# Optimization experiments

Hardware: AMD Instinct MI355X
Metric: run time of the kernel (lower is better)

The kernel has to match this reference:

```python
import jax, jax.numpy as jnp
import numpy as np

B, S, F = 64, 512, 1024
D_MODEL, D_MEM, D_IN, H, D_OUT, N_SYNC, T, H_NLM = 2048, 32, 1024, 16, 1000, 512, 16, 32
DH = D_IN // H


def _ln(x, g, b):
    m = x.mean(-1, keepdims=True)
    v = ((x - m) ** 2).mean(-1, keepdims=True)
    return (x - m) * jax.lax.rsqrt(v + 1e-5) * g + b


def setup_inputs() -> dict:
    key = jax.random.key(0)
    ks = jax.random.split(key, 24)
    def n(i, shape, fan):
        return jax.random.normal(ks[i], shape, jnp.float32) * (fan ** -0.5)
    u = 1.0 / np.sqrt(D_MODEL)
    uh = 1.0 / np.sqrt(D_MODEL + D_MEM)
    return dict(
        x=jax.random.normal(ks[0], (B, S, F), jnp.float32),
        W_kv=n(1, (F, D_IN), F), b_kv=jnp.zeros((D_IN,)),
        g_kv=jnp.ones((D_IN,)), be_kv=jnp.zeros((D_IN,)),
        W_q=n(2, (N_SYNC, D_IN), N_SYNC), b_q=jnp.zeros((D_IN,)),
        W_aq=n(3, (D_IN, D_IN), D_IN), b_aq=jnp.zeros((D_IN,)),
        W_ak=n(4, (D_IN, D_IN), D_IN), b_ak=jnp.zeros((D_IN,)),
        W_av=n(5, (D_IN, D_IN), D_IN), b_av=jnp.zeros((D_IN,)),
        W_ao=n(6, (D_IN, D_IN), D_IN), b_ao=jnp.zeros((D_IN,)),
        W_s1=n(7, (D_IN + D_MODEL, D_MODEL), D_IN + D_MODEL), b_s1=jnp.zeros((D_MODEL,)),
        W_s2=n(8, (D_MODEL, D_MODEL), D_MODEL), b_s2=jnp.zeros((D_MODEL,)),
        g_s=jnp.ones((D_MODEL,)), be_s=jnp.zeros((D_MODEL,)),
        W_n1=n(9, (D_MODEL, D_MEM, H_NLM), D_MEM), b_n1=jnp.zeros((D_MODEL, H_NLM)),
        W_n2=n(10, (D_MODEL, H_NLM), H_NLM), b_n2=jnp.zeros((D_MODEL,)),
        g_n=jnp.ones((D_MODEL,)), be_n=jnp.zeros((D_MODEL,)),
        init_state=jax.random.uniform(ks[11], (D_MODEL,), jnp.float32, -u, u),
        init_hist=jax.random.uniform(ks[12], (D_MODEL, D_MEM), jnp.float32, -uh, uh),
        decay_action=jax.random.uniform(ks[13], (N_SYNC,), jnp.float32, 0.0, 2.0),
        decay_out=jax.random.uniform(ks[14], (N_SYNC,), jnp.float32, 0.0, 2.0),
        W_out=n(15, (N_SYNC, D_OUT), N_SYNC), b_out=jnp.zeros((D_OUT,)),
        idx_la=jax.random.randint(ks[16], (N_SYNC,), 0, D_MODEL),
        idx_ra=jax.random.randint(ks[17], (N_SYNC,), 0, D_MODEL),
        idx_lo=jax.random.randint(ks[18], (N_SYNC,), 0, D_MODEL),
        idx_ro=jax.random.randint(ks[19], (N_SYNC,), 0, D_MODEL),
    )


def reference(x, W_kv, b_kv, g_kv, be_kv, W_q, b_q, W_aq, b_aq, W_ak, b_ak,
              W_av, b_av, W_ao, b_ao, W_s1, b_s1, W_s2, b_s2, g_s, be_s,
              W_n1, b_n1, W_n2, b_n2, g_n, be_n, init_state, init_hist,
              decay_action, decay_out, W_out, b_out,
              idx_la, idx_ra, idx_lo, idx_ro):
    # kv features: Linear + LayerNorm, fixed across ticks -> project k,v once
    kv = _ln(x @ W_kv + b_kv, g_kv, be_kv)                      # (B,S,D_IN)
    kh = (kv @ W_ak + b_ak).reshape(B, S, H, DH)
    vh = (kv @ W_av + b_av).reshape(B, S, H, DH)
    # learnable exponential decay r = exp(-clamp(p,0,15))
    rA = jnp.exp(-jnp.clip(decay_action, 0.0, 15.0))[None, :]
    rO = jnp.exp(-jnp.clip(decay_out, 0.0, 15.0))[None, :]
    act0 = jnp.broadcast_to(init_state, (B, D_MODEL))
    hist0 = jnp.broadcast_to(init_hist, (B, D_MODEL, D_MEM))
    # out-sync initialized before loop (None branch): alpha=prod, beta=1
    aO0 = act0[:, idx_lo] * act0[:, idx_ro]
    bO0 = jnp.ones_like(aO0)
    # action-sync None branch at tick0 == recurrence from alpha=beta=0
    aA0 = jnp.zeros((B, N_SYNC), x.dtype)
    bA0 = jnp.zeros((B, N_SYNC), x.dtype)

    def step(carry, _):
        act, hist, aA, bA, aO, bO = carry
        pA = act[:, idx_la] * act[:, idx_ra]                    # paired-neuron gather
        aA = rA * aA + pA
        bA = rA * bA + 1.0
        sync_a = aA * jax.lax.rsqrt(bA)
        q = sync_a @ W_q + b_q                                  # (B,D_IN)
        qh = (q @ W_aq + b_aq).reshape(B, H, DH)
        attn_w = jax.nn.softmax(jnp.einsum('bhd,bshd->bhs', qh, kh) / np.sqrt(DH), axis=-1)
        attn = jnp.einsum('bhs,bshd->bhd', attn_w, vh).reshape(B, D_IN) @ W_ao + b_ao
        pre = jnp.concatenate([attn, act], axis=-1)             # (B, D_IN+D_MODEL)
        pre_act = _ln(jax.nn.gelu(pre @ W_s1 + b_s1) @ W_s2 + b_s2, g_s, be_s)
        hist = jnp.concatenate([hist[:, :, 1:], pre_act[:, :, None]], axis=-1)
        # per-neuron deep NLM over the memory window
        hmid = jax.nn.relu(jnp.einsum('bdm,dmh->bdh', hist, W_n1) + b_n1)
        act = _ln(jnp.einsum('bdh,dh->bd', hmid, W_n2) + b_n2, g_n, be_n)
        pO = act[:, idx_lo] * act[:, idx_ro]
        aO = rO * aO + pO
        bO = rO * bO + 1.0
        pred = (aO * jax.lax.rsqrt(bO)) @ W_out + b_out         # (B,D_OUT)
        logp = jax.nn.log_softmax(pred, axis=-1)
        ne = -(jnp.exp(logp) * logp).sum(-1) / np.log(D_OUT)    # normalized entropy
        return (act, hist, aA, bA, aO, bO), (pred, ne)

    _, (preds, nes) = jax.lax.scan(step, (act0, hist0, aA0, bA0, aO0, bO0), None, length=T)
    predictions = jnp.transpose(preds, (1, 2, 0))               # (B,D_OUT,T)
    certainties = jnp.transpose(jnp.stack([nes, 1.0 - nes], axis=1), (2, 1, 0))  # (B,2,T)
    return predictions, certainties
```

## Files before the change

kernel.cpp:

```cpp
#include <hip/hip_runtime.h>
#include <hip/hip_bf16.h>


#define B_ 64
#define S_ 512
#define F_ 1024
#define DMODEL 2048
#define DMEM 32
#define DIN 1024
#define NH 16
#define DH 64
#define DOUT 1000
#define NSYNC 512
#define TICKS 16
#define HNLM 32
#define HIST_W 48

typedef __attribute__((ext_vector_type(8))) short short8;
typedef __attribute__((ext_vector_type(4))) float f32x4;

__device__ inline void store_f(float* p, float v) { *p = v; }
__device__ inline void store_f(__hip_bfloat16* p, float v) { *p = __float2bfloat16(v); }

__device__ inline short f2bs(float f) {
  __hip_bfloat16 h = __float2bfloat16(f);
  return *reinterpret_cast<short*>(&h);
}

__device__ inline float bfs(short x) {
  return __uint_as_float(((unsigned)(unsigned short)x) << 16);
}

__device__ inline float gelu_f(float x) {
  float x3 = x * x * x;
  return 0.5f * x * (1.f + tanhf(0.7978845608028654f * (x + 0.044715f * x3)));
}

__device__ inline float bf_lo(unsigned v) { return __uint_as_float(v << 16); }
__device__ inline float bf_hi(unsigned v) { return __uint_as_float(v & 0xffff0000u); }

__global__ __launch_bounds__(256) void transpose_bf16_kernel(const float* __restrict__ W,
                                                             __hip_bfloat16* __restrict__ Wt,
                                                             int K, int N, int Npad, int ldw,
                                                             int koff) {
  __shared__ float t[32][33];
  const int tx = threadIdx.x, ty = threadIdx.y;
  const int n0 = blockIdx.x * 32, k0 = blockIdx.y * 32;
#pragma unroll
  for (int i = 0; i < 4; i++) {
    int k = k0 + ty + i * 8;
    t[ty + i * 8][tx] = (k < K && n0 + tx < N) ? W[(size_t)k * N + n0 + tx] : 0.f;
  }
  __syncthreads();
#pragma unroll
  for (int i = 0; i < 4; i++) {
    int n = n0 + ty + i * 8;
    if (n < Npad && k0 + tx < K)
      Wt[(size_t)n * ldw + koff + k0 + tx] = __float2bfloat16(t[tx][ty + i * 8]);
  }
}

__global__ void conv_bf16_kernel(const float* __restrict__ src, __hip_bfloat16* __restrict__ dst,
                                 int n) {
  int i = blockIdx.x * 256 + threadIdx.x;
  if (i < n) dst[i] = __float2bfloat16(src[i]);
}

__global__ void bqaq_kernel(const float* __restrict__ b_q, const float* __restrict__ b_aq,
                            const __hip_bfloat16* __restrict__ Wt_aq, float* __restrict__ b_qaq) {
  int n = blockIdx.x * 256 + threadIdx.x;
  if (n >= DIN) return;
  const __hip_bfloat16* wr = Wt_aq + (size_t)n * DIN;
  float s = b_aq[n];
  for (int k = 0; k < DIN; k++) s += b_q[k] * __bfloat162float(wr[k]);
  b_qaq[n] = s;
}

__global__ void bs1c_kernel(const float* __restrict__ b_s1, const float* __restrict__ b_ao,
                            const float* __restrict__ W_s1, float* __restrict__ b_s1c) {
  int n = blockIdx.x * 256 + threadIdx.x;
  if (n >= DMODEL) return;
  float s = b_s1[n];
  for (int k = 0; k < DIN; k++) s += b_ao[k] * W_s1[(size_t)k * DMODEL + n];
  b_s1c[n] = s;
}

__device__ inline short8 load_chunk(const __hip_bfloat16* p) {
  return *reinterpret_cast<const short8*>(p);
}
__device__ inline short8 load_chunk(const float* p) {
  short8 r;
#pragma unroll
  for (int j = 0; j < 8; j++) r[j] = f2bs(p[j]);
  return r;
}

template <int TRANSC, typename TA, typename TC>
__global__ __launch_bounds__(256) void gemm_big(const TA* __restrict__ A,
                                                const __hip_bfloat16* __restrict__ Bt,
                                                const float* __restrict__ bias,
                                                TC* __restrict__ C, int M, int N, int K) {
  __shared__ short lsA[128 * 64];
  __shared__ short lsB[128 * 64];
  const int tid = threadIdx.x;
  const int l = tid & 63, w = tid >> 6;
  const int wr = (w >> 1) * 64, wc = (w & 1) * 64;
  const int nwg = gridDim.x * gridDim.y;
  const int flat = blockIdx.y * gridDim.x + blockIdx.x;
  const int wk = (flat & 7) * (nwg >> 3) + (flat >> 3);
  const int brow = (wk / gridDim.x) * 128, bcol = (wk % gridDim.x) * 128;
  f32x4 acc[4][4];
#pragma unroll
  for (int i = 0; i < 4; i++)
#pragma unroll
    for (int j = 0; j < 4; j++)
#pragma unroll
      for (int r = 0; r < 4; r++) acc[i][j][r] = 0.f;

  short8 ra[4], rb[4];
  auto gload = [&](int k0) {
#pragma unroll
    for (int q = 0; q < 4; q++) {
      int i = tid + q * 256;
      int row = i >> 3, c = i & 7;
      ra[q] = load_chunk(A + (size_t)(brow + row) * K + k0 + c * 8);
      rb[q] = load_chunk(Bt + (size_t)(bcol + row) * K + k0 + c * 8);
    }
  };
  auto lwrite = [&]() {
#pragma unroll
    for (int q = 0; q < 4; q++) {
      int i = tid + q * 256;
      int row = i >> 3, c = i & 7;
      int sw = c ^ (row & 7);
      *reinterpret_cast<short8*>(&lsA[row * 64 + sw * 8]) = ra[q];
      *reinterpret_cast<short8*>(&lsB[row * 64 + sw * 8]) = rb[q];
    }
  };
  gload(0);
  for (int k0 = 0; k0 < K; k0 += 64) {
    __syncthreads();
    lwrite();
    if (k0 + 64 < K) gload(k0 + 64);
    __syncthreads();
#pragma unroll
    for (int ks = 0; ks < 2; ks++) {
      short8 af[4], bfv[4];
#pragma unroll
      for (int mi = 0; mi < 4; mi++) {
        int row = wr + mi * 16 + (l & 15);
        int c = ks * 4 + (l >> 4);
        af[mi] = *reinterpret_cast<const short8*>(&lsA[row * 64 + (c ^ (row & 7)) * 8]);
      }
#pragma unroll
      for (int ni = 0; ni < 4; ni++) {
        int row = wc + ni * 16 + (l & 15);
        int c = ks * 4 + (l >> 4);
        bfv[ni] = *reinterpret_cast<const short8*>(&lsB[row * 64 + (c ^ (row & 7)) * 8]);
      }
#pragma unroll
      for (int mi = 0; mi < 4; mi++)
#pragma unroll
        for (int ni = 0; ni < 4; ni++)
          acc[mi][ni] =
              __builtin_amdgcn_mfma_f32_16x16x32_bf16(af[mi], bfv[ni], acc[mi][ni], 0, 0, 0);
    }
  }
#pragma unroll
  for (int mi = 0; mi < 4; mi++)
#pragma unroll
    for (int ni = 0; ni < 4; ni++)
#pragma unroll
      for (int r = 0; r < 4; r++) {
        int row = brow + wr + mi * 16 + (l >> 4) * 4 + r;
        int col = bcol + wc + ni * 16 + (l & 15);
        float v = acc[mi][ni][r];
        if (bias) v += bias[col];
        if (TRANSC == 1) {
          store_f(&C[(size_t)col * M + row], v);
        } else if (TRANSC == 2) {
          int bb = row >> 9, s = row & 511, hh = col >> 6, dd = col & 63;
          store_f(&C[(((size_t)(bb * 16 + hh) * 512) + s) * 64 + dd], v);
        } else {
          store_f(&C[(size_t)row * N + col], v);
        }
      }
}

template <typename TOUT>
__global__ __launch_bounds__(256) void ln_kernel(const float* __restrict__ x,
                                                 const float* __restrict__ g,
                                                 const float* __restrict__ be,
                                                 TOUT* __restrict__ out, int C,
                                                 size_t row_stride, int col_stride) {
  const int row = blockIdx.x;
  const int tid = threadIdx.x;
  const float* xr = x + (size_t)row * C;
  float s = 0.f, s2 = 0.f;
  for (int c = tid; c < C; c += 256) {
    float v = xr[c];
    s += v;
    s2 += v * v;
  }
  __shared__ float r1[256], r2[256];
  r1[tid] = s;
  r2[tid] = s2;
  __syncthreads();
  for (int st = 128; st > 0; st >>= 1) {
    if (tid < st) {
      r1[tid] += r1[tid + st];
      r2[tid] += r2[tid + st];
    }
    __syncthreads();
  }
  float mean = r1[0] / C;
  float var = r2[0] / C - mean * mean;
  float inv = 1.0f / sqrtf(var + 1e-5f);
  for (int c = tid; c < C; c += 256) {
    float v = (xr[c] - mean) * inv * g[c] + be[c];
    store_f(&out[(size_t)row * row_stride + (size_t)c * col_stride], v);
  }
}

__global__ void init_pre_kernel(const float* __restrict__ init_state,
                                __hip_bfloat16* __restrict__ pre) {
  int i = blockIdx.x * 256 + threadIdx.x;
  if (i >= B_ * DMODEL) return;
  int b = i >> 11, j = i & (DMODEL - 1);
  pre[(size_t)b * 3072 + DIN + j] = __float2bfloat16(init_state[j]);
}

__global__ void init_hist_kernel(const float* __restrict__ init_hist, float* __restrict__ hist) {
  int i = blockIdx.x * 256 + threadIdx.x;
  if (i >= B_ * DMODEL * DMEM) return;
  int m = i & (DMEM - 1);
  int bd = i >> 5;
  int d = bd & (DMODEL - 1);
  hist[(size_t)bd * HIST_W + m] = init_hist[d * DMEM + m];
}

__global__ void init_sync_kernel(const float* __restrict__ init_state,
                                 const float* __restrict__ decay_action,
                                 const float* __restrict__ decay_out,
                                 const int* __restrict__ la, const int* __restrict__ ra,
                                 const int* __restrict__ lo, const int* __restrict__ ro,
                                 float* __restrict__ aA, float* __restrict__ bA,
                                 float* __restrict__ aO, float* __restrict__ bO,
                                 float* __restrict__ syncA0, float* __restrict__ rAv,
                                 float* __restrict__ rOv) {
  int i = blockIdx.x * 256 + threadIdx.x;
  if (i >= B_ * NSYNC) return;
  int j = i & (NSYNC - 1);
  if (i < NSYNC) {
    rAv[i] = expf(-fminf(fmaxf(decay_action[i], 0.f), 15.f));
    rOv[i] = expf(-fminf(fmaxf(decay_out[i], 0.f), 15.f));
  }
  float pA = init_state[la[j]] * init_state[ra[j]];
  aA[i] = pA;
  bA[i] = 1.f;
  syncA0[i] = pA;
  aO[i] = init_state[lo[j]] * init_state[ro[j]];
  bO[i] = 1.f;
}

__global__ __launch_bounds__(256) void qh0_kernel(const float* __restrict__ syncA0,
                                                  const __hip_bfloat16* __restrict__ Wt_qaq,
                                                  const float* __restrict__ b_qaq,
                                                  float* __restrict__ qhb) {
  __shared__ float sa[512];
  const int b = blockIdx.x;
  const int tid = threadIdx.x;
  sa[tid] = syncA0[(size_t)b * NSYNC + tid];
  sa[tid + 256] = syncA0[(size_t)b * NSYNC + 256 + tid];
  __syncthreads();
#pragma unroll
  for (int i = 0; i < 4; i++) {
    int n = tid + i * 256;
    const unsigned* wr = reinterpret_cast<const unsigned*>(Wt_qaq + (size_t)n * NSYNC);
    float s = b_qaq[n];
    for (int c = 0; c < 256; c++) {
      unsigned uu = wr[c];
      s += sa[2 * c] * bf_lo(uu) + sa[2 * c + 1] * bf_hi(uu);
    }
    qhb[(size_t)b * DIN + n] = s;
  }
}

template <typename EPI>
__device__ __forceinline__ void mm_tile64(const __hip_bfloat16* __restrict__ A, int lda,
                                          const __hip_bfloat16* __restrict__ Bt, int ldb,
                                          int bcol, int kb, int kchunk, int tid, short* lsA,
                                          short* lsB, EPI epi) {
  const int l = tid & 63, w = tid >> 6;
  f32x4 acc[4];
#pragma unroll
  for (int i = 0; i < 4; i++)
#pragma unroll
    for (int r = 0; r < 4; r++) acc[i][r] = 0.f;
  short8 ra[2], rb[2];
  auto gload = [&](int k0) {
#pragma unroll
    for (int q = 0; q < 2; q++) {
      int i = tid + q * 256;
      int row = i >> 3, c = i & 7;
      ra[q] = *reinterpret_cast<const short8*>(A + (size_t)row * lda + k0 + c * 8);
      rb[q] = *reinterpret_cast<const short8*>(Bt + (size_t)(bcol + row) * ldb + k0 + c * 8);
    }
  };
  auto lwrite = [&]() {
#pragma unroll
    for (int q = 0; q < 2; q++) {
      int i = tid + q * 256;
      int row = i >> 3, c = i & 7;
      int sw = c ^ (row & 7);
      *reinterpret_cast<short8*>(&lsA[row * 64 + sw * 8]) = ra[q];
      *reinterpret_cast<short8*>(&lsB[row * 64 + sw * 8]) = rb[q];
    }
  };
  gload(kb);
  for (int k0 = kb; k0 < kb + kchunk; k0 += 64) {
    __syncthreads();
    lwrite();
    if (k0 + 64 < kb + kchunk) gload(k0 + 64);
    __syncthreads();
#pragma unroll
    for (int ks = 0; ks < 2; ks++) {
      int rowa = w * 16 + (l & 15);
      int c = ks * 4 + (l >> 4);
      short8 af = *reinterpret_cast<const short8*>(&lsA[rowa * 64 + (c ^ (rowa & 7)) * 8]);
#pragma unroll
      for (int ni = 0; ni < 4; ni++) {
        int rowb = ni * 16 + (l & 15);
        short8 bfv = *reinterpret_cast<const short8*>(&lsB[rowb * 64 + (c ^ (rowb & 7)) * 8]);
        acc[ni] = __builtin_amdgcn_mfma_f32_16x16x32_bf16(af, bfv, acc[ni], 0, 0, 0);
      }
    }
  }
#pragma unroll
  for (int ni = 0; ni < 4; ni++)
#pragma unroll
    for (int r = 0; r < 4; r++) {
      int m = w * 16 + (l >> 4) * 4 + r;
      int n = bcol + ni * 16 + (l & 15);
      epi(m, n, acc[ni][r]);
    }
}

__global__ __launch_bounds__(256) void gemm_part(const __hip_bfloat16* __restrict__ A, int lda,
                                                 const __hip_bfloat16* __restrict__ Bt, int ldb,
                                                 float* __restrict__ part, int N, int kchunk) {
  __shared__ short lsA[64 * 64];
  __shared__ short lsB[64 * 64];
  const int tid = threadIdx.x;
  const int nt = blockIdx.x, ks = blockIdx.y;
  mm_tile64(A, lda, Bt, ldb, nt * 64, ks * kchunk, kchunk, tid, lsA, lsB,
            [&](int m, int n, float v) { part[((size_t)(ks * 64 + m)) * N + n] = v; });
}

__global__ void s1_red_kernel(const float* __restrict__ part, const float* __restrict__ bias,
                              __hip_bfloat16* __restrict__ h1, int KS) {
  int i = blockIdx.x * 256 + threadIdx.x;
  int m = i >> 11, n = i & 2047;
  float s = bias[n];
  for (int k = 0; k < KS; k++) s += part[((size_t)(k * 64 + m)) * DMODEL + n];
  h1[(size_t)m * DMODEL + n] = __float2bfloat16(gelu_f(s));
}

__global__ __launch_bounds__(256) void s2_red_ln_kernel(const float* __restrict__ part,
                                                        const float* __restrict__ bias,
                                                        const float* __restrict__ g,
                                                        const float* __restrict__ be,
                                                        float* __restrict__ hist, int KS, int t) {
  __shared__ float r1[256], r2[256];
  const int b = blockIdx.x;
  const int tid = threadIdx.x;
  float v8[8];
  float s = 0.f, s2 = 0.f;
#pragma unroll
  for (int i = 0; i < 8; i++) {
    int n = tid + i * 256;
    float x = bias[n];
    for (int k = 0; k < KS; k++) x += part[((size_t)(k * 64 + b)) * DMODEL + n];
    v8[i] = x;
    s += x;
    s2 += x * x;
  }
  r1[tid] = s;
  r2[tid] = s2;
  __syncthreads();
  for (int st = 128; st > 0; st >>= 1) {
    if (tid < st) {
      r1[tid] += r1[tid + st];
      r2[tid] += r2[tid + st];
    }
    __syncthreads();
  }
  float mean = r1[0] / DMODEL;
  float var = r2[0] / DMODEL - mean * mean;
  float inv = 1.f / sqrtf(var + 1e-5f);
#pragma unroll
  for (int i = 0; i < 8; i++) {
    int n = tid + i * 256;
    float pa = (v8[i] - mean) * inv * g[n] + be[n];
    hist[((size_t)b * DMODEL + n) * HIST_W + 32 + t] = pa;
  }
}

__global__ __launch_bounds__(256) void attn_kernel(const float* __restrict__ qhb,
                                                   const __hip_bfloat16* __restrict__ kh,
                                                   const __hip_bfloat16* __restrict__ vh,
                                                   __hip_bfloat16* __restrict__ pre) {
  __shared__ float qs[64];
  __shared__ float wv[512];
  __shared__ float red[256];
  __shared__ float red2[2048];
  const int u = blockIdx.x;
  const int b = u >> 4, h = u & (NH - 1);
  const int tid = threadIdx.x;
  const __hip_bfloat16* Kp = kh + (size_t)u * (S_ * DH);
  const __hip_bfloat16* Vp = vh + (size_t)u * (S_ * DH);
  if (tid < DH) qs[tid] = qhb[(size_t)b * DIN + h * DH + tid];
  __syncthreads();
  float sc[2];
#pragma unroll
  for (int r = 0; r < 2; ++r) {
    int s = tid + r * 256;
    const short8* kp = reinterpret_cast<const short8*>(Kp + (size_t)s * DH);
    float accv = 0.f;
#pragma unroll
    for (int q = 0; q < 8; ++q) {
      short8 kk = kp[q];
#pragma unroll
      for (int j = 0; j < 8; ++j) accv += qs[q * 8 + j] * bfs(kk[j]);
    }
    sc[r] = accv * 0.125f;
  }
  red[tid] = fmaxf(sc[0], sc[1]);
  __syncthreads();
  for (int st = 128; st > 0; st >>= 1) {
    if (tid < st) red[tid] = fmaxf(red[tid], red[tid + st]);
    __syncthreads();
  }
  const float mx = red[0];
  __syncthreads();
  float e0 = expf(sc[0] - mx), e1 = expf(sc[1] - mx);
  wv[tid] = e0;
  wv[tid + 256] = e1;
  red[tid] = e0 + e1;
  __syncthreads();
  for (int st = 128; st > 0; st >>= 1) {
    if (tid < st) red[tid] += red[tid + st];
    __syncthreads();
  }
  const float invZ = 1.f / red[0];
  __syncthreads();
  const int d8 = tid & 7, sg = tid >> 3;
  float pacc[8];
#pragma unroll
  for (int j = 0; j < 8; ++j) pacc[j] = 0.f;
  for (int s = sg; s < S_; s += 32) {
    float wgt = wv[s];
    short8 vvv = *reinterpret_cast<const short8*>(Vp + (size_t)s * DH + d8 * 8);
#pragma unroll
    for (int j = 0; j < 8; ++j) pacc[j] += wgt * bfs(vvv[j]);
  }
#pragma unroll
  for (int j = 0; j < 8; ++j) red2[sg * 64 + d8 * 8 + j] = pacc[j];
  __syncthreads();
  if (tid < DH) {
    float r = 0.f;
#pragma unroll
    for (int g2 = 0; g2 < 32; ++g2) r += red2[g2 * 64 + tid];
    pre[(size_t)b * 3072 + h * DH + tid] = __float2bfloat16(r * invZ);
  }
}

__global__ __launch_bounds__(256) void nlm_kernel(const float* __restrict__ hist,
                                                  const float* __restrict__ W1,
                                                  const float* __restrict__ b1,
                                                  const float* __restrict__ W2,
                                                  const float* __restrict__ b2,
                                                  float* __restrict__ out, int t) {
  __shared__ float w1s[4096];
  __shared__ float b1s[128];
  const int tid = threadIdx.x;
  const int d0 = blockIdx.x * 4;
  for (int i = tid; i < 4096; i += 256) w1s[i] = W1[(size_t)d0 * 1024 + i];
  if (tid < 128) b1s[tid] = b1[d0 * 32 + tid];
  __syncthreads();
  const int b = tid & 63, dsub = tid >> 6;
  const int d = d0 + dsub;
  const float* hw = hist + ((size_t)(b * DMODEL + d)) * HIST_W + (t + 1);
  float win[DMEM];
#pragma unroll
  for (int m = 0; m < DMEM; ++m) win[m] = hw[m];
  const float* w1 = w1s + dsub * 1024;
  const float* bb = b1s + dsub * 32;
  const float* w2 = W2 + d * HNLM;
  float acc = 0.f;
  for (int h = 0; h < HNLM; ++h) {
    float s = bb[h];
#pragma unroll
    for (int m = 0; m < DMEM; ++m) s += win[m] * w1[m * HNLM + h];
    acc += fmaxf(s, 0.f) * w2[h];
  }
  out[(size_t)b * DMODEL + d] = acc + b2[d];
}

__global__ __launch_bounds__(256) void final_kernel(
    const float* __restrict__ nlmraw, const float* __restrict__ g_n,
    const float* __restrict__ be_n, const int* __restrict__ la, const int* __restrict__ ra,
    const int* __restrict__ lo, const int* __restrict__ ro, const float* __restrict__ rAv,
    const float* __restrict__ rOv, float* __restrict__ aA, float* __restrict__ bA,
    float* __restrict__ aO, float* __restrict__ bO, __hip_bfloat16* __restrict__ pre,
    const __hip_bfloat16* __restrict__ Wt_qaq, const float* __restrict__ b_qaq,
    float* __restrict__ qhb, const __hip_bfloat16* __restrict__ Wt_out,
    const float* __restrict__ b_out, float* __restrict__ outp, int t) {
  __shared__ float arow[2048];
  __shared__ float sa[512];
  __shared__ float so[512];
  __shared__ float pv[1024];
  __shared__ float red[256], red2[256];
  const int b = blockIdx.x;
  const int tid = threadIdx.x;
  const float* xr = nlmraw + (size_t)b * DMODEL;
  float xv[8];
  float s = 0.f, s2 = 0.f;
#pragma unroll
  for (int i = 0; i < 8; i++) {
    float x = xr[tid + i * 256];
    xv[i] = x;
    s += x;
    s2 += x * x;
  }
  red[tid] = s;
  red2[tid] = s2;
  __syncthreads();
  for (int st = 128; st > 0; st >>= 1) {
    if (tid < st) {
      red[tid] += red[tid + st];
      red2[tid] += red2[tid + st];
    }
    __syncthreads();
  }
  float mean = red[0] / DMODEL;
  float var = red2[0] / DMODEL - mean * mean;
  float inv = 1.f / sqrtf(var + 1e-5f);
  __syncthreads();
#pragma unroll
  for (int i = 0; i < 8; i++) {
    int n = tid + i * 256;
    float av = (xv[i] - mean) * inv * g_n[n] + be_n[n];
    arow[n] = av;
    pre[(size_t)b * 3072 + DIN + n] = __float2bfloat16(av);
  }
  __syncthreads();
  for (int j = tid; j < NSYNC; j += 256) {
    size_t idx = (size_t)b * NSYNC + j;
    float pA = arow[la[j]] * arow[ra[j]];
    float r = rAv[j];
    float av2 = r * aA[idx] + pA, bv2 = r * bA[idx] + 1.f;
    aA[idx] = av2;
    bA[idx] = bv2;
    sa[j] = av2 / sqrtf(bv2);
    float pO = arow[lo[j]] * arow[ro[j]];
    float ro2 = rOv[j];
    float av3 = ro2 * aO[idx] + pO, bv3 = ro2 * bO[idx] + 1.f;
    aO[idx] = av3;
    bO[idx] = bv3;
    so[j] = av3 / sqrtf(bv3);
  }
  __syncthreads();
#pragma unroll
  for (int i = 0; i < 4; i++) {
    int n = tid + i * 256;
    const unsigned* wr = reinterpret_cast<const unsigned*>(Wt_qaq + (size_t)n * NSYNC);
    float sacc = b_qaq[n];
    for (int c = 0; c < 256; c++) {
      unsigned uu = wr[c];
      sacc += sa[2 * c] * bf_lo(uu) + sa[2 * c + 1] * bf_hi(uu);
    }
    qhb[(size_t)b * DIN + n] = sacc;
  }
  float pr[4];
#pragma unroll
  for (int i = 0; i < 4; i++) {
    int n = tid + i * 256;
    pr[i] = 0.f;
    if (n < DOUT) {
      const unsigned* wr = reinterpret_cast<const unsigned*>(Wt_out + (size_t)n * NSYNC);
      float sacc = b_out[n];
      for (int c = 0; c < 256; c++) {
        unsigned uu = wr[c];
        sacc += so[2 * c] * bf_lo(uu) + so[2 * c + 1] * bf_hi(uu);
      }
      pr[i] = sacc;
      pv[n] = sacc;
    }
  }
  __syncthreads();
  float m = -1e30f;
  for (int o = tid; o < DOUT; o += 256) m = fmaxf(m, pv[o]);
  red[tid] = m;
  __syncthreads();
  for (int st = 128; st > 0; st >>= 1) {
    if (tid < st) red[tid] = fmaxf(red[tid], red[tid + st]);
    __syncthreads();
  }
  m = red[0];
  __syncthreads();
  float z = 0.f, s1 = 0.f;
  for (int o = tid; o < DOUT; o += 256) {
    float wv2 = pv[o] - m;
    float e = expf(wv2);
    z += e;
    s1 += e * wv2;
  }
  red[tid] = z;
  __syncthreads();
  for (int st = 128; st > 0; st >>= 1) {
    if (tid < st) red[tid] += red[tid + st];
    __syncthreads();
  }
  const float Z = red[0];
  __syncthreads();
  red[tid] = s1;
  __syncthreads();
  for (int st = 128; st > 0; st >>= 1) {
    if (tid < st) red[tid] += red[tid + st];
    __syncthreads();
  }
  const float S1 = red[0];
  const float ne = -(S1 / Z - logf(Z)) / 6.907755278982137f;
#pragma unroll
  for (int i = 0; i < 4; i++) {
    int n = tid + i * 256;
    if (n < DOUT) outp[((size_t)b * DOUT + n) * TICKS + t] = pr[i];
  }
  if (tid == 0) {
    float* c = outp + (size_t)B_ * DOUT * TICKS;
    c[b * 2 * TICKS + t] = ne;
    c[b * 2 * TICKS + TICKS + t] = 1.f - ne;
  }
}

extern "C" void kernel_launch(void* const* d_in, const int* in_sizes, int n_in,
                              void* d_out, int out_size, void* d_ws, size_t ws_size,
                              hipStream_t stream) {
  const float* x = (const float*)d_in[0];
  const float* W_kv = (const float*)d_in[1];
  const float* b_kv = (const float*)d_in[2];
  const float* g_kv = (const float*)d_in[3];
  const float* be_kv = (const float*)d_in[4];
  const float* W_q = (const float*)d_in[5];
  const float* b_q = (const float*)d_in[6];
  const float* W_aq = (const float*)d_in[7];
  const float* b_aq = (const float*)d_in[8];
  const float* W_ak = (const float*)d_in[9];
  const float* b_ak = (const float*)d_in[10];
  const float* W_av = (const float*)d_in[11];
  const float* b_av = (const float*)d_in[12];
  const float* W_ao = (const float*)d_in[13];
  const float* b_ao = (const float*)d_in[14];
  const float* W_s1 = (const float*)d_in[15];
  const float* b_s1 = (const float*)d_in[16];
  const float* W_s2 = (const float*)d_in[17];
  const float* b_s2 = (const float*)d_in[18];
  const float* g_s = (const float*)d_in[19];
  const float* be_s = (const float*)d_in[20];
  const float* W_n1 = (const float*)d_in[21];
  const float* b_n1 = (const float*)d_in[22];
  const float* W_n2 = (const float*)d_in[23];
  const float* b_n2 = (const float*)d_in[24];
  const float* g_n = (const float*)d_in[25];
  const float* be_n = (const float*)d_in[26];
  const float* init_state = (const float*)d_in[27];
  const float* init_hist = (const float*)d_in[28];
  const float* decay_action = (const float*)d_in[29];
  const float* decay_out = (const float*)d_in[30];
  const float* W_out = (const float*)d_in[31];
  const float* b_out = (const float*)d_in[32];
  const int* idx_la = (const int*)d_in[33];
  const int* idx_ra = (const int*)d_in[34];
  const int* idx_lo = (const int*)d_in[35];
  const int* idx_ro = (const int*)d_in[36];
  float* out = (float*)d_out;

  char* wsb = (char*)d_ws;
  size_t off = 0;
  auto alloc = [&](size_t bytes) -> char* {
    char* p = wsb + off;
    off += (bytes + 255) & ~(size_t)255;
    return p;
  };
  const size_t MS = (size_t)B_ * S_;
  char* regionA = alloc(MS * DIN * 4);
  __hip_bfloat16* kv = (__hip_bfloat16*)alloc(MS * DIN * 2);
  float* histf = (float*)alloc((size_t)B_ * DMODEL * HIST_W * 4);
  __hip_bfloat16* Wt_kv = (__hip_bfloat16*)alloc((size_t)DIN * F_ * 2);
  __hip_bfloat16* Wt_ak = (__hip_bfloat16*)alloc((size_t)DIN * DIN * 2);
  __hip_bfloat16* Wt_av = (__hip_bfloat16*)alloc((size_t)DIN * DIN * 2);
  __hip_bfloat16* Wt_aq = (__hip_bfloat16*)alloc((size_t)DIN * DIN * 2);
  __hip_bfloat16* W_ao_b = (__hip_bfloat16*)alloc((size_t)DIN * DIN * 2);
  __hip_bfloat16* W_qb = (__hip_bfloat16*)alloc((size_t)NSYNC * DIN * 2);
  __hip_bfloat16* Wt_qaq = (__hip_bfloat16*)alloc((size_t)DIN * NSYNC * 2);
  __hip_bfloat16* Wts1top = (__hip_bfloat16*)alloc((size_t)DMODEL * DIN * 2);
  __hip_bfloat16* Wt_s1c = (__hip_bfloat16*)alloc((size_t)DMODEL * (DIN + DMODEL) * 2);
  __hip_bfloat16* Wt_s2 = (__hip_bfloat16*)alloc((size_t)DMODEL * DMODEL * 2);
  __hip_bfloat16* Wt_out = (__hip_bfloat16*)alloc((size_t)DOUT * NSYNC * 2);
  float* b_qaq = (float*)alloc(DIN * 4);
  float* b_s1c = (float*)alloc(DMODEL * 4);
  float* partial = (float*)alloc((size_t)8 * 64 * DMODEL * 4);
  float* aA = (float*)alloc((size_t)B_ * NSYNC * 4);
  float* bA = (float*)alloc((size_t)B_ * NSYNC * 4);
  float* aO = (float*)alloc((size_t)B_ * NSYNC * 4);
  float* bO = (float*)alloc((size_t)B_ * NSYNC * 4);
  float* syncA0 = (float*)alloc((size_t)B_ * NSYNC * 4);
  float* qhb = (float*)alloc((size_t)B_ * DIN * 4);
  __hip_bfloat16* pre = (__hip_bfloat16*)alloc((size_t)B_ * (DIN + DMODEL) * 2);
  __hip_bfloat16* h1 = (__hip_bfloat16*)alloc((size_t)B_ * DMODEL * 2);
  float* nlmraw = (float*)alloc((size_t)B_ * DMODEL * 4);
  float* rAv = (float*)alloc(NSYNC * 4);
  float* rOv = (float*)alloc(NSYNC * 4);

  float* kvraw = (float*)regionA;
  __hip_bfloat16* kh = (__hip_bfloat16*)regionA;
  __hip_bfloat16* vh = (__hip_bfloat16*)(regionA + MS * DIN * 2);

  dim3 t32x8(32, 8);
  transpose_bf16_kernel<<<dim3(F_ / 32, DIN / 32), t32x8, 0, stream>>>(W_kv, Wt_kv, F_, DIN, DIN,
                                                                       F_, 0);
  transpose_bf16_kernel<<<dim3(DIN / 32, DIN / 32), t32x8, 0, stream>>>(W_ak, Wt_ak, DIN, DIN,
                                                                        DIN, DIN, 0);
  transpose_bf16_kernel<<<dim3(DIN / 32, DIN / 32), t32x8, 0, stream>>>(W_av, Wt_av, DIN, DIN,
                                                                        DIN, DIN, 0);
  transpose_bf16_kernel<<<dim3(DIN / 32, DIN / 32), t32x8, 0, stream>>>(W_aq, Wt_aq, DIN, DIN,
                                                                        DIN, DIN, 0);
  transpose_bf16_kernel<<<dim3(DMODEL / 32, DIN / 32), t32x8, 0, stream>>>(W_s1, Wts1top, DIN,
                                                                           DMODEL, DMODEL, DIN, 0);
  transpose_bf16_kernel<<<dim3(DMODEL / 32, DMODEL / 32), t32x8, 0, stream>>>(
      W_s1 + (size_t)DIN * DMODEL, Wt_s1c, DMODEL, DMODEL, DMODEL, DIN + DMODEL, DIN);
  transpose_bf16_kernel<<<dim3(DMODEL / 32, DMODEL / 32), t32x8, 0, stream>>>(W_s2, Wt_s2, DMODEL,
                                                                              DMODEL, DMODEL,
                                                                              DMODEL, 0);
  transpose_bf16_kernel<<<dim3((DOUT + 31) / 32, NSYNC / 32), t32x8, 0, stream>>>(
      W_out, Wt_out, NSYNC, DOUT, DOUT, NSYNC, 0);
  conv_bf16_kernel<<<(NSYNC * DIN + 255) / 256, 256, 0, stream>>>(W_q, W_qb, NSYNC * DIN);
  conv_bf16_kernel<<<(DIN * DIN + 255) / 256, 256, 0, stream>>>(W_ao, W_ao_b, DIN * DIN);
  bqaq_kernel<<<4, 256, 0, stream>>>(b_q, b_aq, Wt_aq, b_qaq);
  bs1c_kernel<<<8, 256, 0, stream>>>(b_s1, b_ao, W_s1, b_s1c);

  gemm_big<0, float, float><<<dim3(DIN / 128, MS / 128), 256, 0, stream>>>(x, Wt_kv, b_kv, kvraw,
                                                                           (int)MS, DIN, F_);
  ln_kernel<__hip_bfloat16><<<(int)MS, 256, 0, stream>>>(kvraw, g_kv, be_kv, kv, DIN, DIN, 1);
  gemm_big<2, __hip_bfloat16, __hip_bfloat16><<<dim3(DIN / 128, MS / 128), 256, 0, stream>>>(
      kv, Wt_ak, b_ak, kh, (int)MS, DIN, DIN);
  gemm_big<2, __hip_bfloat16, __hip_bfloat16><<<dim3(DIN / 128, MS / 128), 256, 0, stream>>>(
      kv, Wt_av, b_av, vh, (int)MS, DIN, DIN);
  gemm_big<1, __hip_bfloat16, __hip_bfloat16><<<dim3(DIN / 128, NSYNC / 128), 256, 0, stream>>>(
      W_qb, Wt_aq, nullptr, Wt_qaq, NSYNC, DIN, DIN);
  gemm_big<1, __hip_bfloat16, __hip_bfloat16><<<dim3(DMODEL / 128, DIN / 128), 256, 0, stream>>>(
      W_ao_b, Wts1top, nullptr, Wt_s1c, DIN + DMODEL, DMODEL, DIN);

  init_pre_kernel<<<(B_ * DMODEL + 255) / 256, 256, 0, stream>>>(init_state, pre);
  init_hist_kernel<<<(B_ * DMODEL * DMEM + 255) / 256, 256, 0, stream>>>(init_hist, histf);
  init_sync_kernel<<<(B_ * NSYNC + 255) / 256, 256, 0, stream>>>(
      init_state, decay_action, decay_out, idx_la, idx_ra, idx_lo, idx_ro, aA, bA, aO, bO,
      syncA0, rAv, rOv);
  qh0_kernel<<<B_, 256, 0, stream>>>(syncA0, Wt_qaq, b_qaq, qhb);

  for (int t = 0; t < TICKS; ++t) {
    attn_kernel<<<B_ * NH, 256, 0, stream>>>(qhb, kh, vh, pre);
    gemm_part<<<dim3(32, 8), 256, 0, stream>>>(pre, DIN + DMODEL, Wt_s1c, DIN + DMODEL, partial,
                                               DMODEL, 384);
    s1_red_kernel<<<512, 256, 0, stream>>>(partial, b_s1c, h1, 8);
    gemm_part<<<dim3(32, 8), 256, 0, stream>>>(h1, DMODEL, Wt_s2, DMODEL, partial, DMODEL, 256);
    s2_red_ln_kernel<<<B_, 256, 0, stream>>>(partial, b_s2, g_s, be_s, histf, 8, t);
    nlm_kernel<<<DMODEL / 4, 256, 0, stream>>>(histf, W_n1, b_n1, W_n2, b_n2, nlmraw, t);
    final_kernel<<<B_, 256, 0, stream>>>(nlmraw, g_n, be_n, idx_la, idx_ra, idx_lo, idx_ro, rAv,
                                         rOv, aA, bA, aO, bO, pre, Wt_qaq, b_qaq, qhb, Wt_out,
                                         b_out, out, t);
  }
  (void)in_sizes; (void)n_in; (void)out_size; (void)ws_size;
}
```

Before: 3.191 ms.

## Move synchronisation-query projection to MFMA split-K GEMM and vectorise output projection

```diff
diff --git a/kernel.cpp b/kernel.cpp
--- a/kernel.cpp
+++ b/kernel.cpp
@@ -246,7 +246,7 @@
                                  const int* __restrict__ lo, const int* __restrict__ ro,
                                  float* __restrict__ aA, float* __restrict__ bA,
                                  float* __restrict__ aO, float* __restrict__ bO,
-                                 float* __restrict__ syncA0, float* __restrict__ rAv,
+                                 __hip_bfloat16* __restrict__ syncA, float* __restrict__ rAv,
                                  float* __restrict__ rOv) {
   int i = blockIdx.x * 256 + threadIdx.x;
   if (i >= B_ * NSYNC) return;
@@ -258,32 +258,9 @@
   float pA = init_state[la[j]] * init_state[ra[j]];
   aA[i] = pA;
   bA[i] = 1.f;
-  syncA0[i] = pA;
+  syncA[i] = __float2bfloat16(pA);
   aO[i] = init_state[lo[j]] * init_state[ro[j]];
   bO[i] = 1.f;
-}
-
-__global__ __launch_bounds__(256) void qh0_kernel(const float* __restrict__ syncA0,
-                                                  const __hip_bfloat16* __restrict__ Wt_qaq,
-                                                  const float* __restrict__ b_qaq,
-                                                  float* __restrict__ qhb) {
-  __shared__ float sa[512];
-  const int b = blockIdx.x;
-  const int tid = threadIdx.x;
-  sa[tid] = syncA0[(size_t)b * NSYNC + tid];
-  sa[tid + 256] = syncA0[(size_t)b * NSYNC + 256 + tid];
-  __syncthreads();
-#pragma unroll
-  for (int i = 0; i < 4; i++) {
-    int n = tid + i * 256;
-    const unsigned* wr = reinterpret_cast<const unsigned*>(Wt_qaq + (size_t)n * NSYNC);
-    float s = b_qaq[n];
-    for (int c = 0; c < 256; c++) {
-      unsigned uu = wr[c];
-      s += sa[2 * c] * bf_lo(uu) + sa[2 * c + 1] * bf_hi(uu);
-    }
-    qhb[(size_t)b * DIN + n] = s;
-  }
 }
 
 template <typename EPI>
@@ -406,7 +383,8 @@
   }
 }
 
-__global__ __launch_bounds__(256) void attn_kernel(const float* __restrict__ qhb,
+__global__ __launch_bounds__(256) void attn_kernel(const float* __restrict__ qpart,
+                                                   const float* __restrict__ b_qaq,
                                                    const __hip_bfloat16* __restrict__ kh,
                                                    const __hip_bfloat16* __restrict__ vh,
                                                    __hip_bfloat16* __restrict__ pre) {
@@ -419,7 +397,13 @@
   const int tid = threadIdx.x;
   const __hip_bfloat16* Kp = kh + (size_t)u * (S_ * DH);
   const __hip_bfloat16* Vp = vh + (size_t)u * (S_ * DH);
-  if (tid < DH) qs[tid] = qhb[(size_t)b * DIN + h * DH + tid];
+  if (tid < DH) {
+    int n = h * DH + tid;
+    float s = b_qaq[n];
+#pragma unroll
+    for (int ks = 0; ks < 4; ks++) s += qpart[((size_t)(ks * 64 + b)) * DIN + n];
+    qs[tid] = s;
+  }
   __syncthreads();
   float sc[2];
 #pragma unroll
@@ -512,13 +496,11 @@
     const float* __restrict__ be_n, const int* __restrict__ la, const int* __restrict__ ra,
     const int* __restrict__ lo, const int* __restrict__ ro, const float* __restrict__ rAv,
     const float* __restrict__ rOv, float* __restrict__ aA, float* __restrict__ bA,
-    float* __restrict__ aO, float* __restrict__ bO, __hip_bfloat16* __restrict__ pre,
-    const __hip_bfloat16* __restrict__ Wt_qaq, const float* __restrict__ b_qaq,
-    float* __restrict__ qhb, const __hip_bfloat16* __restrict__ Wt_out,
+    float* __restrict__ aO, float* __restrict__ bO, __hip_bfloat16* __restrict__ syncA,
+    __hip_bfloat16* __restrict__ pre, const __hip_bfloat16* __restrict__ Wt_out,
     const float* __restrict__ b_out, float* __restrict__ outp, int t) {
   __shared__ float arow[2048];
-  __shared__ float sa[512];
-  __shared__ float so[512];
+  __shared__ float so_p[520];
   __shared__ float pv[1024];
   __shared__ float red[256], red2[256];
   const int b = blockIdx.x;
@@ -562,41 +544,33 @@
     float av2 = r * aA[idx] + pA, bv2 = r * bA[idx] + 1.f;
     aA[idx] = av2;
     bA[idx] = bv2;
-    sa[j] = av2 / sqrtf(bv2);
+    syncA[idx] = __float2bfloat16(av2 / sqrtf(bv2));
     float pO = arow[lo[j]] * arow[ro[j]];
     float ro2 = rOv[j];
     float av3 = ro2 * aO[idx] + pO, bv3 = ro2 * bO[idx] + 1.f;
     aO[idx] = av3;
     bO[idx] = bv3;
-    so[j] = av3 / sqrtf(bv3);
-  }
-  __syncthreads();
-#pragma unroll
-  for (int i = 0; i < 4; i++) {
-    int n = tid + i * 256;
-    const unsigned* wr = reinterpret_cast<const unsigned*>(Wt_qaq + (size_t)n * NSYNC);
-    float sacc = b_qaq[n];
-    for (int c = 0; c < 256; c++) {
-      unsigned uu = wr[c];
-      sacc += sa[2 * c] * bf_lo(uu) + sa[2 * c + 1] * bf_hi(uu);
-    }
-    qhb[(size_t)b * DIN + n] = sacc;
-  }
-  float pr[4];
-#pragma unroll
-  for (int i = 0; i < 4; i++) {
-    int n = tid + i * 256;
-    pr[i] = 0.f;
+    so_p[j + (j >> 6)] = av3 / sqrtf(bv3);
+  }
+  __syncthreads();
+  const int lk = tid & 7;
+  const int rg = tid >> 3;
+  for (int it = 0; it < 32; ++it) {
+    int n = it * 32 + rg;
+    float sacc = 0.f;
     if (n < DOUT) {
-      const unsigned* wr = reinterpret_cast<const unsigned*>(Wt_out + (size_t)n * NSYNC);
-      float sacc = b_out[n];
-      for (int c = 0; c < 256; c++) {
-        unsigned uu = wr[c];
-        sacc += so[2 * c] * bf_lo(uu) + so[2 * c + 1] * bf_hi(uu);
+      const short8* wr8 = reinterpret_cast<const short8*>(Wt_out + (size_t)n * NSYNC);
+#pragma unroll
+      for (int q = 0; q < 8; ++q) {
+        short8 w8 = wr8[q * 8 + lk];
+#pragma unroll
+        for (int j = 0; j < 8; ++j) sacc += so_p[q * 65 + lk * 8 + j] * bfs(w8[j]);
       }
-      pr[i] = sacc;
-      pv[n] = sacc;
-    }
+    }
+    sacc += __shfl_xor(sacc, 1);
+    sacc += __shfl_xor(sacc, 2);
+    sacc += __shfl_xor(sacc, 4);
+    if (lk == 0 && n < DOUT) pv[n] = sacc + b_out[n];
   }
   __syncthreads();
   float m = -1e30f;
@@ -632,11 +606,7 @@
   }
   const float S1 = red[0];
   const float ne = -(S1 / Z - logf(Z)) / 6.907755278982137f;
-#pragma unroll
-  for (int i = 0; i < 4; i++) {
-    int n = tid + i * 256;
-    if (n < DOUT) outp[((size_t)b * DOUT + n) * TICKS + t] = pr[i];
-  }
+  for (int o = tid; o < DOUT; o += 256) outp[((size_t)b * DOUT + o) * TICKS + t] = pv[o];
   if (tid == 0) {
     float* c = outp + (size_t)B_ * DOUT * TICKS;
     c[b * 2 * TICKS + t] = ne;
@@ -715,8 +685,7 @@
   float* bA = (float*)alloc((size_t)B_ * NSYNC * 4);
   float* aO = (float*)alloc((size_t)B_ * NSYNC * 4);
   float* bO = (float*)alloc((size_t)B_ * NSYNC * 4);
-  float* syncA0 = (float*)alloc((size_t)B_ * NSYNC * 4);
-  float* qhb = (float*)alloc((size_t)B_ * DIN * 4);
+  __hip_bfloat16* syncA = (__hip_bfloat16*)alloc((size_t)B_ * NSYNC * 2);
   __hip_bfloat16* pre = (__hip_bfloat16*)alloc((size_t)B_ * (DIN + DMODEL) * 2);
   __hip_bfloat16* h1 = (__hip_bfloat16*)alloc((size_t)B_ * DMODEL * 2);
   float* nlmraw = (float*)alloc((size_t)B_ * DMODEL * 4);
@@ -765,12 +734,12 @@
   init_pre_kernel<<<(B_ * DMODEL + 255) / 256, 256, 0, stream>>>(init_state, pre);
   init_hist_kernel<<<(B_ * DMODEL * DMEM + 255) / 256, 256, 0, stream>>>(init_hist, histf);
   init_sync_kernel<<<(B_ * NSYNC + 255) / 256, 256, 0, stream>>>(
-      init_state, decay_action, decay_out, idx_la, idx_ra, idx_lo, idx_ro, aA, bA, aO, bO,
-      syncA0, rAv, rOv);
-  qh0_kernel<<<B_, 256, 0, stream>>>(syncA0, Wt_qaq, b_qaq, qhb);
+      init_state, decay_action, decay_out, idx_la, idx_ra, idx_lo, idx_ro, aA, bA, aO, bO, syncA,
+      rAv, rOv);
 
   for (int t = 0; t < TICKS; ++t) {
-    attn_kernel<<<B_ * NH, 256, 0, stream>>>(qhb, kh, vh, pre);
+    gemm_part<<<dim3(16, 4), 256, 0, stream>>>(syncA, NSYNC, Wt_qaq, NSYNC, partial, DIN, 128);
+    attn_kernel<<<B_ * NH, 256, 0, stream>>>(partial, b_qaq, kh, vh, pre);
     gemm_part<<<dim3(32, 8), 256, 0, stream>>>(pre, DIN + DMODEL, Wt_s1c, DIN + DMODEL, partial,
                                                DMODEL, 384);
     s1_red_kernel<<<512, 256, 0, stream>>>(partial, b_s1c, h1, 8);
@@ -778,8 +747,7 @@
     s2_red_ln_kernel<<<B_, 256, 0, stream>>>(partial, b_s2, g_s, be_s, histf, 8, t);
     nlm_kernel<<<DMODEL / 4, 256, 0, stream>>>(histf, W_n1, b_n1, W_n2, b_n2, nlmraw, t);
     final_kernel<<<B_, 256, 0, stream>>>(nlmraw, g_n, be_n, idx_la, idx_ra, idx_lo, idx_ro, rAv,
-                                         rOv, aA, bA, aO, bO, pre, Wt_qaq, b_qaq, qhb, Wt_out,
-                                         b_out, out, t);
+                                         rOv, aA, bA, aO, bO, syncA, pre, Wt_out, b_out, out, t);
   }
   (void)in_sizes; (void)n_in; (void)out_size; (void)ws_size;
 }
```

New measurement: 2.619 ms. 17.9% less time.
